# Kernel tuning notes

Hardware: AMD Instinct MI355X
Metric: run time of the kernel (lower is better)

Reference implementation:

```python
import jax, jax.numpy as jnp
import numpy as np

N = 100000   # nodes (in_ch)
D = 128      # emb_ch
E = 1600000  # nonzeros in A_hat
RATE = 0.1   # dropout rate


def setup_inputs() -> dict:
    key = jax.random.key(0)
    k1, k2, k3, k4, k5, k6 = jax.random.split(key, 6)
    x = jnp.arange(N, dtype=jnp.int64) if jax.config.jax_enable_x64 else jnp.arange(N, dtype=jnp.int32)
    rows = jax.random.randint(k1, (E,), 0, N)
    cols = jax.random.randint(k2, (E,), 0, N)
    A_vals = jax.random.uniform(k3, (E,), dtype=jnp.float32)
    # xavier_uniform for [N, D]: bound = sqrt(6/(N+D))
    bound = float(np.sqrt(6.0 / (N + D)))
    emb_weight = jax.random.uniform(k4, (N, D), jnp.float32, -bound, bound)
    u1 = jax.random.uniform(k5, (N, D), dtype=jnp.float32)
    u2 = jax.random.uniform(k6, (N, D), dtype=jnp.float32)
    return {"x": x, "rows": rows, "cols": cols, "A_vals": A_vals,
            "emb_weight": emb_weight, "u1": u1, "u2": u2}


def _dropout(h, u):
    keep = (u >= RATE).astype(h.dtype)
    return h * keep / (1.0 - RATE)


def _spmm(rows, cols, vals, h):
    # out[i] = sum_{e: rows[e]==i} vals[e] * h[cols[e]]  -- COO SpMM
    msgs = vals[:, None] * h[cols]  # [E, D]
    return jax.ops.segment_sum(msgs, rows, num_segments=N)


def reference(x, rows, cols, A_vals, emb_weight, u1, u2):
    h0 = emb_weight[x]                       # embedding lookup [N, D]
    h1 = _spmm(rows, cols, A_vals, _dropout(h0, u1))
    h2 = _spmm(rows, cols, A_vals, _dropout(h1, u2))
    return (h0 + h1 + h2) / 3.0
```

## Files before the change

### kernel.cpp

```cpp
#include <hip/hip_runtime.h>
#include <hip/hip_fp16.h>

#define DD 128
#define SCAN_CHUNK 1024
#define G_ROWS 32
#define G_STAGE 1024

typedef float          f32x4 __attribute__((ext_vector_type(4)));
typedef unsigned int   u32x4 __attribute__((ext_vector_type(4)));
typedef unsigned int   u32x2 __attribute__((ext_vector_type(2)));
typedef unsigned short u16x8 __attribute__((ext_vector_type(8)));

struct __align__(8) Edge { int c; float v; };

__device__ __forceinline__ unsigned short f2h(float f) {
    return __half_as_ushort(__float2half(f));
}
__device__ __forceinline__ float2 up2(unsigned int u) {
    __half2 h = *reinterpret_cast<const __half2*>(&u);
    return __half22float2(h);
}

template <typename T>
__device__ __forceinline__ T ldnt(const T* p) { return __builtin_nontemporal_load(p); }
template <typename T>
__device__ __forceinline__ void stnt(T* p, T v) { __builtin_nontemporal_store(v, p); }

__global__ __launch_bounds__(256) void k_g1hist(const float* __restrict__ emb,
                                                const float* __restrict__ u1,
                                                ushort* __restrict__ g1,
                                                const int* __restrict__ rows,
                                                unsigned int* __restrict__ cnt16,
                                                ushort* __restrict__ rank,
                                                int total8, int E) {
    int i = blockIdx.x * 256 + threadIdx.x;
    bool doE = i < E;
    bool doS = i < total8;
    int r = 0;
    if (doE) r = ldnt(rows + i);
    f32x4 hA, hB, uA, uB;
    if (doS) {
        const f32x4* e4 = (const f32x4*)emb;
        const f32x4* a4 = (const f32x4*)u1;
        hA = ldnt(e4 + 2 * (size_t)i);
        hB = ldnt(e4 + 2 * (size_t)i + 1);
        uA = ldnt(a4 + 2 * (size_t)i);
        uB = ldnt(a4 + 2 * (size_t)i + 1);
    }
    if (doE) {
        int sh = (r & 1) << 4;
        unsigned int old = atomicAdd(&cnt16[r >> 1], 1u << sh);
        stnt(rank + i, (ushort)((old >> sh) & 0xFFFFu));
    }
    if (doS) {
        const float s = 1.0f / 0.9f;
        u16x8 g;
        g[0] = f2h((uA.x >= 0.1f) ? hA.x * s : 0.0f);
        g[1] = f2h((uA.y >= 0.1f) ? hA.y * s : 0.0f);
        g[2] = f2h((uA.z >= 0.1f) ? hA.z * s : 0.0f);
        g[3] = f2h((uA.w >= 0.1f) ? hA.w * s : 0.0f);
        g[4] = f2h((uB.x >= 0.1f) ? hB.x * s : 0.0f);
        g[5] = f2h((uB.y >= 0.1f) ? hB.y * s : 0.0f);
        g[6] = f2h((uB.z >= 0.1f) ? hB.z * s : 0.0f);
        g[7] = f2h((uB.w >= 0.1f) ? hB.w * s : 0.0f);
        ((u16x8*)g1)[i] = g;
    }
}

__global__ __launch_bounds__(256) void k_scan1(const unsigned int* __restrict__ cnt16,
                                               int* __restrict__ rs,
                                               int* __restrict__ bsum, int n) {
    __shared__ int s[256];
    int tid = threadIdx.x;
    int base = blockIdx.x * SCAN_CHUNK + tid * 4;
    int c0 = 0, c1 = 0, c2 = 0, c3 = 0;
    if (base < n) {
        unsigned int w0 = cnt16[base >> 1];
        c0 = (int)(w0 & 0xFFFFu);
        c1 = (int)(w0 >> 16);
    }
    if (base + 2 < n) {
        unsigned int w1 = cnt16[(base >> 1) + 1];
        c2 = (int)(w1 & 0xFFFFu);
        c3 = (int)(w1 >> 16);
    }
    int tsum = c0 + c1 + c2 + c3;
    s[tid] = tsum;
    __syncthreads();
    for (int off = 1; off < 256; off <<= 1) {
        int t = (tid >= off) ? s[tid - off] : 0;
        __syncthreads();
        s[tid] += t;
        __syncthreads();
    }
    int excl = s[tid] - tsum;
    if (tid == 255) bsum[blockIdx.x] = s[255];
    if (base < n)     rs[base]     = excl;
    if (base + 1 < n) rs[base + 1] = excl + c0;
    if (base + 2 < n) rs[base + 2] = excl + c0 + c1;
    if (base + 3 < n) rs[base + 3] = excl + c0 + c1 + c2;
}

__global__ __launch_bounds__(256) void k_scan23(int* __restrict__ rs,
                                                const int* __restrict__ bsum,
                                                int nb, int n) {
    __shared__ int s[1024];
    int tid = threadIdx.x;
    for (int i = tid; i < nb; i += 256) s[i] = bsum[i];
    __syncthreads();
    if (tid == 0) {
        int run = 0;
        for (int i = 0; i < nb; ++i) { int t = s[i]; s[i] = run; run += t; }
    }
    __syncthreads();
    int i = blockIdx.x * 256 + tid;
    if (i < n) rs[i] += s[i >> 10];
}

__global__ __launch_bounds__(256) void k_scatter_prep(const int* __restrict__ rows,
                                                      const int* __restrict__ cols,
                                                      const float* __restrict__ vals,
                                                      const int* __restrict__ rs,
                                                      const ushort* __restrict__ rank,
                                                      Edge* __restrict__ ev,
                                                      const float* __restrict__ emb,
                                                      const float* __restrict__ u2,
                                                      ushort* __restrict__ emb16,
                                                      unsigned char* __restrict__ mask2,
                                                      int E, int total8) {
    int i = blockIdx.x * 256 + threadIdx.x;
    bool doE = i < E;
    bool doS = i < total8;
    int r = 0, c = 0; float vv = 0.f; unsigned int rk = 0;
    if (doE) {
        r = ldnt(rows + i);
        c = ldnt(cols + i);
        vv = ldnt(vals + i);
        rk = ldnt(rank + i);
    }
    f32x4 hA, hB, vA, vB;
    if (doS) {
        const f32x4* e4 = (const f32x4*)emb;
        const f32x4* b4 = (const f32x4*)u2;
        hA = ldnt(e4 + 2 * (size_t)i);
        hB = ldnt(e4 + 2 * (size_t)i + 1);
        vA = ldnt(b4 + 2 * (size_t)i);
        vB = ldnt(b4 + 2 * (size_t)i + 1);
    }
    if (doE) {
        int pos = rs[r] + (int)rk;
        u32x2 q;
        q.x = (unsigned int)c;
        q.y = __float_as_uint(vv);
        ((u32x2*)ev)[pos] = q;
    }
    if (doS) {
        u16x8 e16;
        e16[0] = f2h(hA.x); e16[1] = f2h(hA.y); e16[2] = f2h(hA.z); e16[3] = f2h(hA.w);
        e16[4] = f2h(hB.x); e16[5] = f2h(hB.y); e16[6] = f2h(hB.z); e16[7] = f2h(hB.w);
        stnt((u16x8*)emb16 + i, e16);
        unsigned char m =
            (unsigned char)((vA.x >= 0.1f ? 1u : 0u)  | (vA.y >= 0.1f ? 2u : 0u)  |
                            (vA.z >= 0.1f ? 4u : 0u)  | (vA.w >= 0.1f ? 8u : 0u)  |
                            (vB.x >= 0.1f ? 16u : 0u) | (vB.y >= 0.1f ? 32u : 0u) |
                            (vB.z >= 0.1f ? 64u : 0u) | (vB.w >= 0.1f ? 128u : 0u));
        stnt(mask2 + i, m);
    }
}

template <int MODE>
__global__ __launch_bounds__(256, 4) void k_gather(const int* __restrict__ rowstart,
                                                   const Edge* __restrict__ ev,
                                                   const ushort* __restrict__ srch,
                                                   const unsigned char* __restrict__ mask2,
                                                   const ushort* __restrict__ emb16,
                                                   const ushort* __restrict__ p16in,
                                                   ushort* __restrict__ p16out,
                                                   ushort* __restrict__ g2,
                                                   float* __restrict__ out,
                                                   int N, int E) {
    __shared__ int s_rs[G_ROWS + 1];
    __shared__ Edge s_ev[G_STAGE];

    int tid = threadIdx.x;
    int r0 = blockIdx.x * G_ROWS;
    int h = blockIdx.y;
    if (tid <= G_ROWS) {
        int r = r0 + tid;
        s_rs[tid] = (r < N) ? rowstart[r] : E;
    }
    __syncthreads();
    int base = s_rs[0];
    int nblk = s_rs[G_ROWS] - base;
    int nstage = nblk < G_STAGE ? nblk : G_STAGE;
    for (int i = tid; i < nstage; i += 256) {
        u32x2 q = ldnt((const u32x2*)(ev + base + i));
        Edge ed; ed.c = (int)q.x; ed.v = __uint_as_float(q.y);
        s_ev[i] = ed;
    }
    __syncthreads();

    int grp = tid >> 3;
    int lane = tid & 7;
    int row = r0 + grp;
    if (row >= N) return;
    int start = s_rs[grp] - base;
    int end = s_rs[grp + 1] - base;
    int eL = end < nstage ? end : nstage;

    const u32x4* __restrict__ s4 = (const u32x4*)srch;
    const Edge* __restrict__ evg = ev + base;
    int hoff = (h << 3) + lane;
    float a0 = 0.f, a1 = 0.f, a2 = 0.f, a3 = 0.f;
    float a4 = 0.f, a5 = 0.f, a6 = 0.f, a7 = 0.f;

#define LDE(i) Edge E##i = s_ev[e + i]; float fv##i = E##i.v;
#define LDP(i) int ix##i = e + i; bool ok##i = ix##i < eL; \
               Edge E##i = s_ev[ok##i ? ix##i : last]; \
               float fv##i = ok##i ? E##i.v : 0.0f;
#define GQ(i)  u32x4 q##i = s4[((size_t)E##i.c << 4) + hoff];
#define ACC(i) { float vv = fv##i; \
        float2 w0 = up2(q##i.x), w1 = up2(q##i.y), w2 = up2(q##i.z), w3 = up2(q##i.w); \
        a0 = fmaf(vv, w0.x, a0); a1 = fmaf(vv, w0.y, a1); \
        a2 = fmaf(vv, w1.x, a2); a3 = fmaf(vv, w1.y, a3); \
        a4 = fmaf(vv, w2.x, a4); a5 = fmaf(vv, w2.y, a5); \
        a6 = fmaf(vv, w3.x, a6); a7 = fmaf(vv, w3.y, a7); }

    int e = start;
    for (; e + 16 <= eL; e += 16) {
        LDE(0)  LDE(1)  LDE(2)  LDE(3)  LDE(4)  LDE(5)  LDE(6)  LDE(7)
        LDE(8)  LDE(9)  LDE(10) LDE(11) LDE(12) LDE(13) LDE(14) LDE(15)
        GQ(0)  GQ(1)  GQ(2)  GQ(3)  GQ(4)  GQ(5)  GQ(6)  GQ(7)
        GQ(8)  GQ(9)  GQ(10) GQ(11) GQ(12) GQ(13) GQ(14) GQ(15)
        ACC(0)  ACC(1)  ACC(2)  ACC(3)  ACC(4)  ACC(5)  ACC(6)  ACC(7)
        ACC(8)  ACC(9)  ACC(10) ACC(11) ACC(12) ACC(13) ACC(14) ACC(15)
    }
    if (e < eL) {
        int last = eL - 1;
        LDP(0)  LDP(1)  LDP(2)  LDP(3)  LDP(4)  LDP(5)  LDP(6)  LDP(7)
        LDP(8)  LDP(9)  LDP(10) LDP(11) LDP(12) LDP(13) LDP(14) LDP(15)
        GQ(0)  GQ(1)  GQ(2)  GQ(3)  GQ(4)  GQ(5)  GQ(6)  GQ(7)
        GQ(8)  GQ(9)  GQ(10) GQ(11) GQ(12) GQ(13) GQ(14) GQ(15)
        ACC(0)  ACC(1)  ACC(2)  ACC(3)  ACC(4)  ACC(5)  ACC(6)  ACC(7)
        ACC(8)  ACC(9)  ACC(10) ACC(11) ACC(12) ACC(13) ACC(14) ACC(15)
        e = eL;
    }
    for (; e < end; ++e) {
        Edge E0; { u32x2 q_ = ldnt((const u32x2*)(evg + e));
                   E0.c = (int)q_.x; E0.v = __uint_as_float(q_.y); }
        float fv0 = E0.v;
        GQ(0) ACC(0)
    }
#undef LDE
#undef LDP
#undef GQ
#undef ACC

    size_t o = ((size_t)row << 7) + ((size_t)h << 6) + (size_t)lane * 8;
    if (MODE == 1) {
        unsigned int m = mask2[(size_t)row * 16 + (h << 3) + lane];
        const float s = 1.0f / 0.9f;
        u16x8 gg;
        gg[0] = (m & 1u)   ? f2h(a0 * s) : (ushort)0;
        gg[1] = (m & 2u)   ? f2h(a1 * s) : (ushort)0;
        gg[2] = (m & 4u)   ? f2h(a2 * s) : (ushort)0;
        gg[3] = (m & 8u)   ? f2h(a3 * s) : (ushort)0;
        gg[4] = (m & 16u)  ? f2h(a4 * s) : (ushort)0;
        gg[5] = (m & 32u)  ? f2h(a5 * s) : (ushort)0;
        gg[6] = (m & 64u)  ? f2h(a6 * s) : (ushort)0;
        gg[7] = (m & 128u) ? f2h(a7 * s) : (ushort)0;
        stnt((u16x8*)(g2 + o), gg);
        u16x8 pp;
        pp[0] = f2h(a0); pp[1] = f2h(a1); pp[2] = f2h(a2); pp[3] = f2h(a3);
        pp[4] = f2h(a4); pp[5] = f2h(a5); pp[6] = f2h(a6); pp[7] = f2h(a7);
        stnt((u16x8*)(p16out + o), pp);
    } else {
        u32x4 eq = ldnt((const u32x4*)(emb16 + o));
        u32x4 pq = ldnt((const u32x4*)(p16in + o));
        float2 e0 = up2(eq.x), e1 = up2(eq.y), e2 = up2(eq.z), e3 = up2(eq.w);
        float2 p0 = up2(pq.x), p1 = up2(pq.y), p2 = up2(pq.z), p3 = up2(pq.w);
        const float t3 = 1.0f / 3.0f;
        f32x4 rA, rB;
        rA.x = (e0.x + p0.x + a0) * t3;
        rA.y = (e0.y + p0.y + a1) * t3;
        rA.z = (e1.x + p1.x + a2) * t3;
        rA.w = (e1.y + p1.y + a3) * t3;
        rB.x = (e2.x + p2.x + a4) * t3;
        rB.y = (e2.y + p2.y + a5) * t3;
        rB.z = (e3.x + p3.x + a6) * t3;
        rB.w = (e3.y + p3.y + a7) * t3;
        stnt((f32x4*)(out + o), rA);
        stnt((f32x4*)(out + o) + 1, rB);
    }
}


extern "C" void kernel_launch(void* const* d_in, const int* in_sizes, int n_in,
                              void* d_out, int out_size, void* d_ws, size_t ws_size,
                              hipStream_t stream) {
    const int* rows = (const int*)d_in[1];
    const int* cols = (const int*)d_in[2];
    const float* vals = (const float*)d_in[3];
    const float* emb = (const float*)d_in[4];
    const float* u1 = (const float*)d_in[5];
    const float* u2 = (const float*)d_in[6];
    float* out = (float*)d_out;

    const int N = in_sizes[0];
    const int E = in_sizes[1];
    const size_t ND = (size_t)N * DD;
    const int NW = (N + 1) / 2;

    char* ws = (char*)d_ws;
    Edge* ev     = (Edge*)ws;   ws += (size_t)E * sizeof(Edge);
    ushort* g1   = (ushort*)ws; ws += ND * sizeof(ushort);
    ushort* g2   = (ushort*)ws; ws += ND * sizeof(ushort);
    ushort* p16  = (ushort*)ws; ws += ND * sizeof(ushort);
    ushort* emb16= (ushort*)ws; ws += ND * sizeof(ushort);
    unsigned int* cnt16 = (unsigned int*)ws; ws += (size_t)NW * 4;
    int* rs      = (int*)ws;    ws += (size_t)N * sizeof(int);
    ushort* rank = (ushort*)ws; ws += (size_t)E * sizeof(ushort);
    int* bsum    = (int*)ws;    ws += 4096;
    unsigned char* mask2 = (unsigned char*)ws;

    const int total8 = (int)(ND / 8);
    const int prepBlocks = (total8 + 255) / 256;
    const int gridE = (E + 255) / 256;
    const int gridFuse = prepBlocks > gridE ? prepBlocks : gridE;
    const int nScanBlocks = (N + SCAN_CHUNK - 1) / SCAN_CHUNK;
    const int gridRowX = (N + G_ROWS - 1) / G_ROWS;
    dim3 gridRow(gridRowX, 2, 1);

    hipMemsetAsync(cnt16, 0, (size_t)NW * 4, stream);
    k_g1hist<<<gridFuse, 256, 0, stream>>>(emb, u1, g1, rows, cnt16, rank,
                                           total8, E);
    k_scan1<<<nScanBlocks, 256, 0, stream>>>(cnt16, rs, bsum, N);
    k_scan23<<<(N + 255) / 256, 256, 0, stream>>>(rs, bsum, nScanBlocks, N);
    k_scatter_prep<<<gridFuse, 256, 0, stream>>>(rows, cols, vals, rs, rank,
                                                 ev, emb, u2, emb16, mask2,
                                                 E, total8);
    k_gather<1><<<gridRow, 256, 0, stream>>>(rs, ev, g1, mask2, nullptr, nullptr,
                                             p16, g2, nullptr, N, E);
    k_gather<2><<<gridRow, 256, 0, stream>>>(rs, ev, g2, nullptr, emb16, p16,
                                             nullptr, nullptr, out, N, E);
}
```

Before: 404.3 us.

## Fuse scan stages via last-block prefix and process two items per thread

Drops the separate block-sum scan-and-add kernel. The last scan block to finish, found with an atomic counter and a threadfence, computes the block prefixes into a small array. Consumers (scatter and gather) then add pref[r>>10] at read time instead of rewriting rs. The histogram and scatter-prep kernels also handle two elements per thread with half the grid, to raise memory-level parallelism. One kernel launch is saved, at the cost of an extra indirection read in the consumers and a serial prefix loop in a single block.

Measured after the change: 410.3 us. About the same (+1.5%).

```diff
diff --git a/kernel.cpp b/kernel.cpp
--- a/kernel.cpp
+++ b/kernel.cpp
@@ -25,6 +25,21 @@
 __device__ __forceinline__ T ldnt(const T* p) { return __builtin_nontemporal_load(p); }
 template <typename T>
 __device__ __forceinline__ void stnt(T* p, T v) { __builtin_nontemporal_store(v, p); }
+
+__device__ __forceinline__ u16x8 drop8(const f32x4& hA, const f32x4& hB,
+                                       const f32x4& uA, const f32x4& uB) {
+    const float s = 1.0f / 0.9f;
+    u16x8 g;
+    g[0] = f2h((uA.x >= 0.1f) ? hA.x * s : 0.0f);
+    g[1] = f2h((uA.y >= 0.1f) ? hA.y * s : 0.0f);
+    g[2] = f2h((uA.z >= 0.1f) ? hA.z * s : 0.0f);
+    g[3] = f2h((uA.w >= 0.1f) ? hA.w * s : 0.0f);
+    g[4] = f2h((uB.x >= 0.1f) ? hB.x * s : 0.0f);
+    g[5] = f2h((uB.y >= 0.1f) ? hB.y * s : 0.0f);
+    g[6] = f2h((uB.z >= 0.1f) ? hB.z * s : 0.0f);
+    g[7] = f2h((uB.w >= 0.1f) ? hB.w * s : 0.0f);
+    return g;
+}
 
 __global__ __launch_bounds__(256) void k_g1hist(const float* __restrict__ emb,
                                                 const float* __restrict__ u1,
@@ -33,46 +48,50 @@
                                                 unsigned int* __restrict__ cnt16,
                                                 ushort* __restrict__ rank,
                                                 int total8, int E) {
-    int i = blockIdx.x * 256 + threadIdx.x;
-    bool doE = i < E;
-    bool doS = i < total8;
-    int r = 0;
-    if (doE) r = ldnt(rows + i);
-    f32x4 hA, hB, uA, uB;
-    if (doS) {
-        const f32x4* e4 = (const f32x4*)emb;
-        const f32x4* a4 = (const f32x4*)u1;
-        hA = ldnt(e4 + 2 * (size_t)i);
-        hB = ldnt(e4 + 2 * (size_t)i + 1);
-        uA = ldnt(a4 + 2 * (size_t)i);
-        uB = ldnt(a4 + 2 * (size_t)i + 1);
-    }
-    if (doE) {
-        int sh = (r & 1) << 4;
-        unsigned int old = atomicAdd(&cnt16[r >> 1], 1u << sh);
-        stnt(rank + i, (ushort)((old >> sh) & 0xFFFFu));
-    }
-    if (doS) {
-        const float s = 1.0f / 0.9f;
-        u16x8 g;
-        g[0] = f2h((uA.x >= 0.1f) ? hA.x * s : 0.0f);
-        g[1] = f2h((uA.y >= 0.1f) ? hA.y * s : 0.0f);
-        g[2] = f2h((uA.z >= 0.1f) ? hA.z * s : 0.0f);
-        g[3] = f2h((uA.w >= 0.1f) ? hA.w * s : 0.0f);
-        g[4] = f2h((uB.x >= 0.1f) ? hB.x * s : 0.0f);
-        g[5] = f2h((uB.y >= 0.1f) ? hB.y * s : 0.0f);
-        g[6] = f2h((uB.z >= 0.1f) ? hB.z * s : 0.0f);
-        g[7] = f2h((uB.w >= 0.1f) ? hB.w * s : 0.0f);
-        ((u16x8*)g1)[i] = g;
-    }
+    int i0 = blockIdx.x * 512 + threadIdx.x;
+    int i1 = i0 + 256;
+    bool dE0 = i0 < E,      dE1 = i1 < E;
+    bool dS0 = i0 < total8, dS1 = i1 < total8;
+    int r0 = 0, r1 = 0;
+    if (dE0) r0 = ldnt(rows + i0);
+    if (dE1) r1 = ldnt(rows + i1);
+    f32x4 hA0, hB0, uA0, uB0, hA1, hB1, uA1, uB1;
+    const f32x4* e4 = (const f32x4*)emb;
+    const f32x4* a4 = (const f32x4*)u1;
+    if (dS0) {
+        hA0 = ldnt(e4 + 2 * (size_t)i0);
+        hB0 = ldnt(e4 + 2 * (size_t)i0 + 1);
+        uA0 = ldnt(a4 + 2 * (size_t)i0);
+        uB0 = ldnt(a4 + 2 * (size_t)i0 + 1);
+    }
+    if (dS1) {
+        hA1 = ldnt(e4 + 2 * (size_t)i1);
+        hB1 = ldnt(e4 + 2 * (size_t)i1 + 1);
+        uA1 = ldnt(a4 + 2 * (size_t)i1);
+        uB1 = ldnt(a4 + 2 * (size_t)i1 + 1);
+    }
+    unsigned int o0 = 0, o1 = 0;
+    int sh0 = (r0 & 1) << 4, sh1 = (r1 & 1) << 4;
+    if (dE0) o0 = atomicAdd(&cnt16[r0 >> 1], 1u << sh0);
+    if (dE1) o1 = atomicAdd(&cnt16[r1 >> 1], 1u << sh1);
+    if (dE0) stnt(rank + i0, (ushort)((o0 >> sh0) & 0xFFFFu));
+    if (dE1) stnt(rank + i1, (ushort)((o1 >> sh1) & 0xFFFFu));
+    if (dS0) ((u16x8*)g1)[i0] = drop8(hA0, hB0, uA0, uB0);
+    if (dS1) ((u16x8*)g1)[i1] = drop8(hA1, hB1, uA1, uB1);
 }
 
 __global__ __launch_bounds__(256) void k_scan1(const unsigned int* __restrict__ cnt16,
                                                int* __restrict__ rs,
-                                               int* __restrict__ bsum, int n) {
+                                               int* __restrict__ bsum,
+                                               int* __restrict__ pref,
+                                               int* __restrict__ done,
+                                               int n, int nb) {
     __shared__ int s[256];
+    __shared__ int sL[1024];
+    __shared__ int lastFlag;
     int tid = threadIdx.x;
-    int base = blockIdx.x * SCAN_CHUNK + tid * 4;
+    int b = blockIdx.x;
+    int base = b * SCAN_CHUNK + tid * 4;
     int c0 = 0, c1 = 0, c2 = 0, c3 = 0;
     if (base < n) {
         unsigned int w0 = cnt16[base >> 1];
@@ -94,33 +113,32 @@
         __syncthreads();
     }
     int excl = s[tid] - tsum;
-    if (tid == 255) bsum[blockIdx.x] = s[255];
     if (base < n)     rs[base]     = excl;
     if (base + 1 < n) rs[base + 1] = excl + c0;
     if (base + 2 < n) rs[base + 2] = excl + c0 + c1;
     if (base + 3 < n) rs[base + 3] = excl + c0 + c1 + c2;
-}
-
-__global__ __launch_bounds__(256) void k_scan23(int* __restrict__ rs,
-                                                const int* __restrict__ bsum,
-                                                int nb, int n) {
-    __shared__ int s[1024];
-    int tid = threadIdx.x;
-    for (int i = tid; i < nb; i += 256) s[i] = bsum[i];
+    if (tid == 255) {
+        atomicAdd(&bsum[b], s[255]);
+        __threadfence();
+        int old = atomicAdd(done, 1);
+        lastFlag = (old == nb - 1) ? 1 : 0;
+    }
     __syncthreads();
-    if (tid == 0) {
-        int run = 0;
-        for (int i = 0; i < nb; ++i) { int t = s[i]; s[i] = run; run += t; }
-    }
-    __syncthreads();
-    int i = blockIdx.x * 256 + tid;
-    if (i < n) rs[i] += s[i >> 10];
+    if (lastFlag) {
+        for (int i = tid; i < nb; i += 256) sL[i] = atomicAdd(&bsum[i], 0);
+        __syncthreads();
+        if (tid == 0) {
+            int run = 0;
+            for (int i = 0; i < nb; ++i) { int t = sL[i]; pref[i] = run; run += t; }
+        }
+    }
 }
 
 __global__ __launch_bounds__(256) void k_scatter_prep(const int* __restrict__ rows,
                                                       const int* __restrict__ cols,
                                                       const float* __restrict__ vals,
                                                       const int* __restrict__ rs,
+                                                      const int* __restrict__ pref,
                                                       const ushort* __restrict__ rank,
                                                       Edge* __restrict__ ev,
                                                       const float* __restrict__ emb,
@@ -128,48 +146,75 @@
                                                       ushort* __restrict__ emb16,
                                                       unsigned char* __restrict__ mask2,
                                                       int E, int total8) {
-    int i = blockIdx.x * 256 + threadIdx.x;
-    bool doE = i < E;
-    bool doS = i < total8;
-    int r = 0, c = 0; float vv = 0.f; unsigned int rk = 0;
-    if (doE) {
-        r = ldnt(rows + i);
-        c = ldnt(cols + i);
-        vv = ldnt(vals + i);
-        rk = ldnt(rank + i);
-    }
-    f32x4 hA, hB, vA, vB;
-    if (doS) {
-        const f32x4* e4 = (const f32x4*)emb;
-        const f32x4* b4 = (const f32x4*)u2;
-        hA = ldnt(e4 + 2 * (size_t)i);
-        hB = ldnt(e4 + 2 * (size_t)i + 1);
-        vA = ldnt(b4 + 2 * (size_t)i);
-        vB = ldnt(b4 + 2 * (size_t)i + 1);
-    }
-    if (doE) {
-        int pos = rs[r] + (int)rk;
-        u32x2 q;
-        q.x = (unsigned int)c;
-        q.y = __float_as_uint(vv);
+    int i0 = blockIdx.x * 512 + threadIdx.x;
+    int i1 = i0 + 256;
+    bool dE0 = i0 < E,      dE1 = i1 < E;
+    bool dS0 = i0 < total8, dS1 = i1 < total8;
+    int r0 = 0, c0 = 0, r1 = 0, c1 = 0;
+    float v0 = 0.f, v1 = 0.f;
+    unsigned int k0 = 0, k1 = 0;
+    if (dE0) {
+        r0 = ldnt(rows + i0); c0 = ldnt(cols + i0);
+        v0 = ldnt(vals + i0); k0 = ldnt(rank + i0);
+    }
+    if (dE1) {
+        r1 = ldnt(rows + i1); c1 = ldnt(cols + i1);
+        v1 = ldnt(vals + i1); k1 = ldnt(rank + i1);
+    }
+    f32x4 hA0, hB0, wA0, wB0, hA1, hB1, wA1, wB1;
+    const f32x4* e4 = (const f32x4*)emb;
+    const f32x4* b4 = (const f32x4*)u2;
+    if (dS0) {
+        hA0 = ldnt(e4 + 2 * (size_t)i0);
+        hB0 = ldnt(e4 + 2 * (size_t)i0 + 1);
+        wA0 = ldnt(b4 + 2 * (size_t)i0);
+        wB0 = ldnt(b4 + 2 * (size_t)i0 + 1);
+    }
+    if (dS1) {
+        hA1 = ldnt(e4 + 2 * (size_t)i1);
+        hB1 = ldnt(e4 + 2 * (size_t)i1 + 1);
+        wA1 = ldnt(b4 + 2 * (size_t)i1);
+        wB1 = ldnt(b4 + 2 * (size_t)i1 + 1);
+    }
+    if (dE0) {
+        int pos = rs[r0] + pref[r0 >> 10] + (int)k0;
+        u32x2 q; q.x = (unsigned int)c0; q.y = __float_as_uint(v0);
         ((u32x2*)ev)[pos] = q;
     }
-    if (doS) {
+    if (dE1) {
+        int pos = rs[r1] + pref[r1 >> 10] + (int)k1;
+        u32x2 q; q.x = (unsigned int)c1; q.y = __float_as_uint(v1);
+        ((u32x2*)ev)[pos] = q;
+    }
+    if (dS0) {
         u16x8 e16;
-        e16[0] = f2h(hA.x); e16[1] = f2h(hA.y); e16[2] = f2h(hA.z); e16[3] = f2h(hA.w);
-        e16[4] = f2h(hB.x); e16[5] = f2h(hB.y); e16[6] = f2h(hB.z); e16[7] = f2h(hB.w);
-        stnt((u16x8*)emb16 + i, e16);
+        e16[0] = f2h(hA0.x); e16[1] = f2h(hA0.y); e16[2] = f2h(hA0.z); e16[3] = f2h(hA0.w);
+        e16[4] = f2h(hB0.x); e16[5] = f2h(hB0.y); e16[6] = f2h(hB0.z); e16[7] = f2h(hB0.w);
+        stnt((u16x8*)emb16 + i0, e16);
         unsigned char m =
-            (unsigned char)((vA.x >= 0.1f ? 1u : 0u)  | (vA.y >= 0.1f ? 2u : 0u)  |
-                            (vA.z >= 0.1f ? 4u : 0u)  | (vA.w >= 0.1f ? 8u : 0u)  |
-                            (vB.x >= 0.1f ? 16u : 0u) | (vB.y >= 0.1f ? 32u : 0u) |
-                            (vB.z >= 0.1f ? 64u : 0u) | (vB.w >= 0.1f ? 128u : 0u));
-        stnt(mask2 + i, m);
+            (unsigned char)((wA0.x >= 0.1f ? 1u : 0u)  | (wA0.y >= 0.1f ? 2u : 0u)  |
+                            (wA0.z >= 0.1f ? 4u : 0u)  | (wA0.w >= 0.1f ? 8u : 0u)  |
+                            (wB0.x >= 0.1f ? 16u : 0u) | (wB0.y >= 0.1f ? 32u : 0u) |
+                            (wB0.z >= 0.1f ? 64u : 0u) | (wB0.w >= 0.1f ? 128u : 0u));
+        stnt(mask2 + i0, m);
+    }
+    if (dS1) {
+        u16x8 e16;
+        e16[0] = f2h(hA1.x); e16[1] = f2h(hA1.y); e16[2] = f2h(hA1.z); e16[3] = f2h(hA1.w);
+        e16[4] = f2h(hB1.x); e16[5] = f2h(hB1.y); e16[6] = f2h(hB1.z); e16[7] = f2h(hB1.w);
+        stnt((u16x8*)emb16 + i1, e16);
+        unsigned char m =
+            (unsigned char)((wA1.x >= 0.1f ? 1u : 0u)  | (wA1.y >= 0.1f ? 2u : 0u)  |
+                            (wA1.z >= 0.1f ? 4u : 0u)  | (wA1.w >= 0.1f ? 8u : 0u)  |
+                            (wB1.x >= 0.1f ? 16u : 0u) | (wB1.y >= 0.1f ? 32u : 0u) |
+                            (wB1.z >= 0.1f ? 64u : 0u) | (wB1.w >= 0.1f ? 128u : 0u));
+        stnt(mask2 + i1, m);
     }
 }
 
 template <int MODE>
-__global__ __launch_bounds__(256, 4) void k_gather(const int* __restrict__ rowstart,
+__global__ __launch_bounds__(256, 4) void k_gather(const int* __restrict__ rs,
+                                                   const int* __restrict__ pref,
                                                    const Edge* __restrict__ ev,
                                                    const ushort* __restrict__ srch,
                                                    const unsigned char* __restrict__ mask2,
@@ -187,7 +232,7 @@
     int h = blockIdx.y;
     if (tid <= G_ROWS) {
         int r = r0 + tid;
-        s_rs[tid] = (r < N) ? rowstart[r] : E;
+        s_rs[tid] = (r < N) ? (rs[r] + pref[r >> 10]) : E;
     }
     __syncthreads();
     int base = s_rs[0];
@@ -318,29 +363,30 @@
     ushort* p16  = (ushort*)ws; ws += ND * sizeof(ushort);
     ushort* emb16= (ushort*)ws; ws += ND * sizeof(ushort);
     unsigned int* cnt16 = (unsigned int*)ws; ws += (size_t)NW * 4;
+    int* bsum    = (int*)ws;    ws += 4096;
+    int* done    = (int*)ws;    ws += 64;
+    int* pref    = (int*)ws;    ws += 4096;
     int* rs      = (int*)ws;    ws += (size_t)N * sizeof(int);
     ushort* rank = (ushort*)ws; ws += (size_t)E * sizeof(ushort);
-    int* bsum    = (int*)ws;    ws += 4096;
     unsigned char* mask2 = (unsigned char*)ws;
 
     const int total8 = (int)(ND / 8);
-    const int prepBlocks = (total8 + 255) / 256;
-    const int gridE = (E + 255) / 256;
-    const int gridFuse = prepBlocks > gridE ? prepBlocks : gridE;
+    const int dom = total8 > E ? total8 : E;
+    const int gridFuse = (dom + 511) / 512;
     const int nScanBlocks = (N + SCAN_CHUNK - 1) / SCAN_CHUNK;
     const int gridRowX = (N + G_ROWS - 1) / G_ROWS;
     dim3 gridRow(gridRowX, 2, 1);
 
-    hipMemsetAsync(cnt16, 0, (size_t)NW * 4, stream);
+    hipMemsetAsync(cnt16, 0, (size_t)NW * 4 + 4096 + 64, stream);
     k_g1hist<<<gridFuse, 256, 0, stream>>>(emb, u1, g1, rows, cnt16, rank,
                                            total8, E);
-    k_scan1<<<nScanBlocks, 256, 0, stream>>>(cnt16, rs, bsum, N);
-    k_scan23<<<(N + 255) / 256, 256, 0, stream>>>(rs, bsum, nScanBlocks, N);
-    k_scatter_prep<<<gridFuse, 256, 0, stream>>>(rows, cols, vals, rs, rank,
+    k_scan1<<<nScanBlocks, 256, 0, stream>>>(cnt16, rs, bsum, pref, done,
+                                             N, nScanBlocks);
+    k_scatter_prep<<<gridFuse, 256, 0, stream>>>(rows, cols, vals, rs, pref, rank,
                                                  ev, emb, u2, emb16, mask2,
                                                  E, total8);
-    k_gather<1><<<gridRow, 256, 0, stream>>>(rs, ev, g1, mask2, nullptr, nullptr,
-                                             p16, g2, nullptr, N, E);
-    k_gather<2><<<gridRow, 256, 0, stream>>>(rs, ev, g2, nullptr, emb16, p16,
-                                             nullptr, nullptr, out, N, E);
-}
+    k_gather<1><<<gridRow, 256, 0, stream>>>(rs, pref, ev, g1, mask2, nullptr,
+                                             nullptr, p16, g2, nullptr, N, E);
+    k_gather<2><<<gridRow, 256, 0, stream>>>(rs, pref, ev, g2, nullptr, emb16,
+                                             p16, nullptr, nullptr, out, N, E);
+}
```
